# Optimization experiments

Hardware: AMD Instinct MI355X
Metric: run time of the kernel (lower is better)

## Reference

```python
import jax, jax.numpy as jnp
import numpy as np

NUM_HEADS = 16
HEAD_DIM = 64
BATCH = 4
SEQ = 1024
MAX_SEQ_LEN = 2048


def _shift(pos_score):
    # Transformer-XL relative shift. pos_score: (NH, S, S_kv)
    NH, S, S_kv = pos_score.shape
    zero_pad = jnp.zeros((NH, S, 1), dtype=pos_score.dtype)
    padded = jnp.concatenate([zero_pad, pos_score], axis=-1)  # (NH, S, S_kv+1)
    padded = padded.reshape(NH, S_kv + 1, S)
    return padded[:, 1:, :].reshape(NH, S, S_kv)


def setup_inputs() -> dict:
    key = jax.random.key(0)
    ks = jax.random.split(key, 6)
    NH = BATCH * NUM_HEADS
    return {
        "queries": jax.random.normal(ks[0], (NH, SEQ, HEAD_DIM), dtype=jnp.float32),
        "keys": jax.random.normal(ks[1], (NH, SEQ, HEAD_DIM), dtype=jnp.float32),
        "values": jax.random.normal(ks[2], (NH, SEQ, HEAD_DIM), dtype=jnp.float32),
        "u_bias": jax.random.normal(ks[3], (1, NUM_HEADS, 1, HEAD_DIM), dtype=jnp.float32),
        "v_bias": jax.random.normal(ks[4], (1, NUM_HEADS, 1, HEAD_DIM), dtype=jnp.float32),
        "R": jax.random.normal(ks[5], (NUM_HEADS, MAX_SEQ_LEN, HEAD_DIM), dtype=jnp.float32),
    }


def reference(queries, keys, values, u_bias, v_bias, R):
    NH, S, d = queries.shape
    S_kv = keys.shape[1]
    batch = NH // NUM_HEADS

    q = queries * (d ** -0.5)
    q = q.reshape(batch, NUM_HEADS, S, d)
    q_u = (q + u_bias).reshape(NH, S, d)
    q_v = (q + v_bias).reshape(NH, S, d)

    # relative position embeddings, tiled over batch: (NH, S_kv, d)
    R_s = jnp.tile(R[:, :S_kv, :], (batch, 1, 1))

    content_score = jnp.einsum('nsd,ntd->nst', q_u, keys)   # (NH, S, S_kv)
    pos_score = jnp.einsum('nsd,ntd->nst', q_v, R_s)        # (NH, S, S_kv)
    pos_score = _shift(pos_score)

    attn_weights = jax.nn.softmax(content_score + pos_score, axis=-1)
    attn = jnp.einsum('nst,ntd->nsd', attn_weights, values)  # (NH, S, d)
    return attn
```

## Files before the change

kernel.cpp:

```cpp
#include <hip/hip_runtime.h>


#define SQ    1024
#define HD    64
#define NHD   16
#define RMAX  2048

typedef _Float16 f16x8 __attribute__((ext_vector_type(8)));
typedef _Float16 f16x4 __attribute__((ext_vector_type(4)));
typedef short    b16x8 __attribute__((ext_vector_type(8)));
typedef float    f32x4 __attribute__((ext_vector_type(4)));

#define MFMA_F16(A,B,C)  __builtin_amdgcn_mfma_f32_16x16x32_f16((A),(B),(C),0,0,0)
#define MFMA_BF16(A,B,C) __builtin_amdgcn_mfma_f32_16x16x32_bf16((A),(B),(C),0,0,0)

#define KH_OFF   0
#define VT_OFF   (8u << 20)
#define R16_OFF  (18u << 20)
#define WS_NEED  (20u << 20)

__device__ __forceinline__ short f2b(float f) {
  unsigned u = __builtin_bit_cast(unsigned, f);
  u += 0x7FFFu + ((u >> 16) & 1u);
  return (short)(u >> 16);
}
__device__ __forceinline__ unsigned pkh(float a, float b) {
  _Float16 h0 = (_Float16)a, h1 = (_Float16)b;
  return (unsigned)__builtin_bit_cast(unsigned short, h0)
       | ((unsigned)__builtin_bit_cast(unsigned short, h1) << 16);
}


__global__ __launch_bounds__(256) void precvt_kr(
    const float* __restrict__ K, const float* __restrict__ R,
    _Float16* __restrict__ Kh, _Float16* __restrict__ R16)
{
  const int idx = blockIdx.x * 256 + threadIdx.x;
  const int nk4 = (64 * SQ * HD) / 4;
  if (idx < nk4) {
    float4 v = ((const float4*)K)[idx];
    f16x4 o = { (_Float16)v.x, (_Float16)v.y, (_Float16)v.z, (_Float16)v.w };
    *(f16x4*)(Kh + 4 * (size_t)idx) = o;
  } else {
    int rr = idx - nk4;
    int h  = rr >> 14, off = rr & 16383;
    float4 v = ((const float4*)R)[((size_t)h << 15) + off];
    f16x4 o = { (_Float16)v.x, (_Float16)v.y, (_Float16)v.z, (_Float16)v.w };
    *(f16x4*)(R16 + 4 * (((size_t)h << 14) + off)) = o;
  }
}

__global__ __launch_bounds__(256) void prevt_v(
    const float* __restrict__ V, short* __restrict__ Vt)
{
  __shared__ float t[64][65];
  const int n = blockIdx.x, st = blockIdx.y, tid = threadIdx.x;
  {
    const int row = tid >> 2, c0 = (tid & 3) * 16;
    const float* src = V + ((size_t)n * SQ + st * 64 + row) * HD + c0;
#pragma unroll
    for (int i = 0; i < 4; ++i) {
      float4 x = ((const float4*)src)[i];
      t[row][c0 + 4*i + 0] = x.x; t[row][c0 + 4*i + 1] = x.y;
      t[row][c0 + 4*i + 2] = x.z; t[row][c0 + 4*i + 3] = x.w;
    }
  }
  __syncthreads();
  {
    const int d = tid >> 2, s0 = (tid & 3) * 16;
    short* dst = Vt + ((size_t)n * 80 + d) * SQ + st * 64 + s0;
#pragma unroll
    for (int i = 0; i < 8; ++i) {
      unsigned pk = (unsigned)(unsigned short)f2b(t[s0 + 2*i][d])
                  | ((unsigned)(unsigned short)f2b(t[s0 + 2*i + 1][d]) << 16);
      *(unsigned*)(dst + 2*i) = pk;
    }
  }
  if (tid < 64) {
    const int s = st * 64 + tid;
    Vt[((size_t)n * 80 + 64) * SQ + s] = (short)0x3F80;
#pragma unroll
    for (int r = 65; r < 80; ++r) Vt[((size_t)n * 80 + r) * SQ + s] = 0;
  }
}


__global__ __launch_bounds__(256, 4) void relpos_sdpa_r5(
    const float* __restrict__ Q, const _Float16* __restrict__ Kh,
    const short* __restrict__ Vtg, const _Float16* __restrict__ R16,
    const float* __restrict__ Ub, const float* __restrict__ Vb,
    float* __restrict__ O)
{
  const int n    = blockIdx.x;
  const int h    = n & (NHD - 1);
  const int a0   = blockIdx.y * 64;
  const int tid  = threadIdx.x;
  const int lane = tid & 63, wave = tid >> 6;
  const int l15  = lane & 15, quad = lane >> 4;

  const float*    Qn  = Q   + (size_t)n * SQ * HD;
  const _Float16* Khn = Kh  + (size_t)n * SQ * HD;
  const short*    Vgn = Vtg + (size_t)n * 80 * SQ;
  const _Float16* Rh  = R16 + (size_t)h * SQ * HD;

  __shared__ __align__(16) char lds[38656];
  _Float16* Kb = (_Float16*)lds;
  short*    Ps = (short*)lds;
  short*    Vt = (short*)(lds + 9216);
  _Float16* Pb = (_Float16*)(lds + 9216 + 11520);

  f16x8 quF[2], qvF[5][2];
#pragma unroll
  for (int ks = 0; ks < 2; ++ks) {
    const int db = ks * 32 + quad * 8;
    float ub[8], vb[8];
#pragma unroll
    for (int j = 0; j < 8; ++j) { ub[j] = Ub[h*HD + db + j]; vb[j] = Vb[h*HD + db + j]; }
    {
      const float* p = Qn + (size_t)(a0 + 16*wave + l15) * HD + db;
      f16x8 f;
#pragma unroll
      for (int j = 0; j < 8; ++j) f[j] = (_Float16)(p[j] * 0.125f + ub[j]);
      quF[ks] = f;
    }
#pragma unroll
    for (int rt = 0; rt < 5; ++rt) {
      int row = a0 + 16*rt + l15; if (row > SQ-1) row = SQ-1;
      const float* p = Qn + (size_t)row * HD + db;
      f16x8 f;
#pragma unroll
      for (int j = 0; j < 8; ++j) f[j] = (_Float16)(p[j] * 0.125f + vb[j]);
      qvF[rt][ks] = f;
    }
  }

  if (tid < 64) Vt[64*72 + tid] = (short)0x3F80;

  f32x4 Oacc[5];
#pragma unroll
  for (int ct = 0; ct < 5; ++ct) Oacc[ct] = (f32x4){0.f, 0.f, 0.f, 0.f};

  auto band = [&](int jstart) {
    const int c    = jstart + 16*wave + l15;
    const int j    = (c + 2048) & (SQ - 1);
    const int slot = (c + 2048) & 127;
    const _Float16* rp = Rh + (size_t)j * HD + quad * 8;
    f16x8 B0 = *(const f16x8*)rp;
    f16x8 B1 = *(const f16x8*)(rp + 32);
#pragma unroll
    for (int rt = 0; rt < 5; ++rt) {
      f32x4 acc = (f32x4){0.f, 0.f, 0.f, 0.f};
      acc = MFMA_F16(qvF[rt][0], B0, acc);
      acc = MFMA_F16(qvF[rt][1], B1, acc);
      const int row = 16*rt + 4*quad;
      if (rt < 4) {
        *(unsigned*)&Pb[slot*70 + row]     = pkh(acc[0], acc[1]);
        *(unsigned*)&Pb[slot*70 + row + 2] = pkh(acc[2], acc[3]);
      } else if (quad == 0) {
        *(unsigned*)&Pb[slot*70 + row]     = pkh(acc[0], acc[1]);
      }
    }
  };

  band(-a0 - 65);
  band(-a0 - 1);

  const int sr = tid >> 2, sc4 = tid & 3;
  const int iiB = 16*wave + 4*quad;

  for (int k0 = 0; k0 < SQ; k0 += 64) {
    __syncthreads();

    {
      const _Float16* src = Khn + (size_t)(k0 + sr) * HD + sc4 * 16;
      *(f16x8*)&Kb[sr*72 + sc4*16]     = *(const f16x8*)src;
      *(f16x8*)&Kb[sr*72 + sc4*16 + 8] = *(const f16x8*)(src + 8);
    }
    {
      const short* src = Vgn + (size_t)sr * SQ + k0 + sc4 * 16;
      *(b16x8*)&Vt[sr*72 + sc4*16]     = *(const b16x8*)src;
      *(b16x8*)&Vt[sr*72 + sc4*16 + 8] = *(const b16x8*)(src + 8);
    }
    __syncthreads();

    f32x4 sc[4];
#pragma unroll
    for (int ct = 0; ct < 4; ++ct) {
      f16x8 b0 = *(const f16x8*)&Kb[(16*ct + l15)*72 + quad*8];
      f16x8 b1 = *(const f16x8*)&Kb[(16*ct + l15)*72 + 32 + quad*8];
      f32x4 acc = (f32x4){0.f, 0.f, 0.f, 0.f};
      acc = MFMA_F16(quF[0], b0, acc);
      acc = MFMA_F16(quF[1], b1, acc);
      sc[ct] = acc;
    }

    const int dlt = k0 - a0;
#pragma unroll
    for (int r = 0; r < 4; ++r) {
      const int ii = iiB + r;
#pragma unroll
      for (int ct = 0; ct < 4; ++ct) {
        const int e    = dlt + 16*ct + l15 - ii;
        const int u    = (e > 0) ? 1 : 0;
        const int slot = (e - 1 - u + 2048) & 127;
        float pos = (float)Pb[slot*70 + ii + u];
        float s   = sc[ct][r] + ((e == 1) ? 0.f : pos);
        sc[ct][r] = __expf(s - 40.0f);
      }
    }
    __syncthreads();

#pragma unroll
    for (int r = 0; r < 4; ++r)
#pragma unroll
      for (int ct = 0; ct < 4; ++ct)
        Ps[(iiB + r)*68 + 16*ct + l15] = f2b(sc[ct][r]);

    b16x8 pA0 = *(const b16x8*)&Ps[(16*wave + l15)*68 + quad*8];
    b16x8 pA1 = *(const b16x8*)&Ps[(16*wave + l15)*68 + 32 + quad*8];
#pragma unroll
    for (int ct = 0; ct < 5; ++ct) {
      b16x8 v0 = *(const b16x8*)&Vt[(16*ct + l15)*72 + quad*8];
      b16x8 v1 = *(const b16x8*)&Vt[(16*ct + l15)*72 + 32 + quad*8];
      Oacc[ct] = MFMA_BF16(pA0, v0, Oacc[ct]);
      Oacc[ct] = MFMA_BF16(pA1, v1, Oacc[ct]);
    }

    if (k0 < SQ - 64) band(k0 + 64 - a0 - 1);
  }

#pragma unroll
  for (int r = 0; r < 4; ++r) {
    float l   = __shfl(Oacc[4][r], lane & 48);
    float inv = 1.0f / l;
    const size_t rowo = (size_t)n * SQ * HD + (size_t)(a0 + iiB + r) * HD;
#pragma unroll
    for (int ct = 0; ct < 4; ++ct)
      O[rowo + 16*ct + l15] = Oacc[ct][r] * inv;
  }
}


__global__ __launch_bounds__(256, 4) void relpos_sdpa_r3(
    const float* __restrict__ Q, const float* __restrict__ K,
    const float* __restrict__ V, const float* __restrict__ Ub,
    const float* __restrict__ Vb, const float* __restrict__ R,
    float* __restrict__ O)
{
  const int n    = blockIdx.x;
  const int h    = n & (NHD - 1);
  const int a0   = blockIdx.y * 64;
  const int tid  = threadIdx.x;
  const int lane = tid & 63, wave = tid >> 6;
  const int l15  = lane & 15, quad = lane >> 4;

  const float* Qn = Q + (size_t)n * SQ * HD;
  const float* Kn = K + (size_t)n * SQ * HD;
  const float* Vn = V + (size_t)n * SQ * HD;
  const float* Rh = R + (size_t)h * RMAX * HD;

  __shared__ __align__(16) char lds[38656];
  _Float16* Kb = (_Float16*)lds;
  short*    Ps = (short*)lds;
  short*    Vt = (short*)(lds + 9216);
  _Float16* Pb = (_Float16*)(lds + 9216 + 11520);

  f16x8 quF[2], qvF[5][2];
#pragma unroll
  for (int ks = 0; ks < 2; ++ks) {
    const int db = ks * 32 + quad * 8;
    float ub[8], vb[8];
#pragma unroll
    for (int j = 0; j < 8; ++j) { ub[j] = Ub[h*HD + db + j]; vb[j] = Vb[h*HD + db + j]; }
    {
      const float* p = Qn + (size_t)(a0 + 16*wave + l15) * HD + db;
      f16x8 f;
#pragma unroll
      for (int j = 0; j < 8; ++j) f[j] = (_Float16)(p[j] * 0.125f + ub[j]);
      quF[ks] = f;
    }
#pragma unroll
    for (int rt = 0; rt < 5; ++rt) {
      int row = a0 + 16*rt + l15; if (row > SQ-1) row = SQ-1;
      const float* p = Qn + (size_t)row * HD + db;
      f16x8 f;
#pragma unroll
      for (int j = 0; j < 8; ++j) f[j] = (_Float16)(p[j] * 0.125f + vb[j]);
      qvF[rt][ks] = f;
    }
  }

  if (tid < 64) Vt[64*72 + tid] = (short)0x3F80;

  f32x4 Oacc[5];
#pragma unroll
  for (int ct = 0; ct < 5; ++ct) Oacc[ct] = (f32x4){0.f, 0.f, 0.f, 0.f};

  auto band = [&](int jstart) {
    const int c    = jstart + 16*wave + l15;
    const int j    = (c + 2048) & (SQ - 1);
    const int slot = (c + 2048) & 127;
    const float* rp = Rh + (size_t)j * HD + quad * 8;
    f16x8 B0, B1;
    {
      float4 x0 = *(const float4*)(rp),      x1 = *(const float4*)(rp + 4);
      float4 y0 = *(const float4*)(rp + 32), y1 = *(const float4*)(rp + 36);
#pragma unroll
      for (int t = 0; t < 4; ++t) { B0[t] = (_Float16)(&x0.x)[t]; B0[t+4] = (_Float16)(&x1.x)[t]; }
#pragma unroll
      for (int t = 0; t < 4; ++t) { B1[t] = (_Float16)(&y0.x)[t]; B1[t+4] = (_Float16)(&y1.x)[t]; }
    }
#pragma unroll
    for (int rt = 0; rt < 5; ++rt) {
      f32x4 acc = (f32x4){0.f, 0.f, 0.f, 0.f};
      acc = MFMA_F16(qvF[rt][0], B0, acc);
      acc = MFMA_F16(qvF[rt][1], B1, acc);
      const int row = 16*rt + 4*quad;
      if (rt < 4) {
        *(unsigned*)&Pb[slot*70 + row]     = pkh(acc[0], acc[1]);
        *(unsigned*)&Pb[slot*70 + row + 2] = pkh(acc[2], acc[3]);
      } else if (quad == 0) {
        *(unsigned*)&Pb[slot*70 + row]     = pkh(acc[0], acc[1]);
      }
    }
  };

  band(-a0 - 65);
  band(-a0 - 1);

  const int sr = tid >> 2, sc4 = tid & 3;
  const int iiB = 16*wave + 4*quad;

  for (int k0 = 0; k0 < SQ; k0 += 64) {
    __syncthreads();
    {
      const float* src = Kn + (size_t)(k0 + sr) * HD + sc4 * 16;
      float4 x0 = *(const float4*)(src),     x1 = *(const float4*)(src + 4);
      float4 y0 = *(const float4*)(src + 8), y1 = *(const float4*)(src + 12);
      f16x8 lo, hi;
#pragma unroll
      for (int t = 0; t < 4; ++t) { lo[t] = (_Float16)(&x0.x)[t]; lo[t+4] = (_Float16)(&x1.x)[t]; }
#pragma unroll
      for (int t = 0; t < 4; ++t) { hi[t] = (_Float16)(&y0.x)[t]; hi[t+4] = (_Float16)(&y1.x)[t]; }
      *(f16x8*)&Kb[sr*72 + sc4*16]     = lo;
      *(f16x8*)&Kb[sr*72 + sc4*16 + 8] = hi;
    }
    {
      const int g = lane >> 3;
#pragma unroll
      for (int i = 0; i < 8; ++i) {
        int bp = 8*wave + (i ^ g);
        float v0 = Vn[(size_t)(k0 + 2*bp)     * HD + lane];
        float v1 = Vn[(size_t)(k0 + 2*bp + 1) * HD + lane];
        unsigned pk = (unsigned)(unsigned short)f2b(v0)
                    | ((unsigned)(unsigned short)f2b(v1) << 16);
        *(unsigned*)&Vt[lane*72 + 2*bp] = pk;
      }
    }
    __syncthreads();

    f32x4 sc[4];
#pragma unroll
    for (int ct = 0; ct < 4; ++ct) {
      f16x8 b0 = *(const f16x8*)&Kb[(16*ct + l15)*72 + quad*8];
      f16x8 b1 = *(const f16x8*)&Kb[(16*ct + l15)*72 + 32 + quad*8];
      f32x4 acc = (f32x4){0.f, 0.f, 0.f, 0.f};
      acc = MFMA_F16(quF[0], b0, acc);
      acc = MFMA_F16(quF[1], b1, acc);
      sc[ct] = acc;
    }

    const int dlt = k0 - a0;
#pragma unroll
    for (int r = 0; r < 4; ++r) {
      const int ii = iiB + r;
#pragma unroll
      for (int ct = 0; ct < 4; ++ct) {
        const int e    = dlt + 16*ct + l15 - ii;
        const int u    = (e > 0) ? 1 : 0;
        const int slot = (e - 1 - u + 2048) & 127;
        float pos = (float)Pb[slot*70 + ii + u];
        float s   = sc[ct][r] + ((e == 1) ? 0.f : pos);
        sc[ct][r] = __expf(s - 40.0f);
      }
    }
    __syncthreads();

#pragma unroll
    for (int r = 0; r < 4; ++r)
#pragma unroll
      for (int ct = 0; ct < 4; ++ct)
        Ps[(iiB + r)*68 + 16*ct + l15] = f2b(sc[ct][r]);

    b16x8 pA0 = *(const b16x8*)&Ps[(16*wave + l15)*68 + quad*8];
    b16x8 pA1 = *(const b16x8*)&Ps[(16*wave + l15)*68 + 32 + quad*8];
#pragma unroll
    for (int ct = 0; ct < 5; ++ct) {
      b16x8 v0 = *(const b16x8*)&Vt[(16*ct + l15)*72 + quad*8];
      b16x8 v1 = *(const b16x8*)&Vt[(16*ct + l15)*72 + 32 + quad*8];
      Oacc[ct] = MFMA_BF16(pA0, v0, Oacc[ct]);
      Oacc[ct] = MFMA_BF16(pA1, v1, Oacc[ct]);
    }

    if (k0 < SQ - 64) band(k0 + 64 - a0 - 1);
  }

#pragma unroll
  for (int r = 0; r < 4; ++r) {
    float l   = __shfl(Oacc[4][r], lane & 48);
    float inv = 1.0f / l;
    const size_t rowo = (size_t)n * SQ * HD + (size_t)(a0 + iiB + r) * HD;
#pragma unroll
    for (int ct = 0; ct < 4; ++ct)
      O[rowo + 16*ct + l15] = Oacc[ct][r] * inv;
  }
}

extern "C" void kernel_launch(void* const* d_in, const int* in_sizes, int n_in,
                              void* d_out, int out_size, void* d_ws, size_t ws_size,
                              hipStream_t stream) {
  const float* Q  = (const float*)d_in[0];
  const float* K  = (const float*)d_in[1];
  const float* V  = (const float*)d_in[2];
  const float* Ub = (const float*)d_in[3];
  const float* Vb = (const float*)d_in[4];
  const float* R  = (const float*)d_in[5];
  float* O = (float*)d_out;

  if (ws_size >= WS_NEED) {
    _Float16* Kh  = (_Float16*)((char*)d_ws + KH_OFF);
    short*    Vt  = (short*)((char*)d_ws + VT_OFF);
    _Float16* R16 = (_Float16*)((char*)d_ws + R16_OFF);

    precvt_kr<<<5120, 256, 0, stream>>>(K, R, Kh, R16);
    prevt_v<<<dim3(64, 16), 256, 0, stream>>>(V, Vt);

    dim3 grid(64, 16);
    relpos_sdpa_r5<<<grid, 256, 0, stream>>>(Q, Kh, Vt, R16, Ub, Vb, O);
  } else {
    dim3 grid(64, 16);
    relpos_sdpa_r3<<<grid, 256, 0, stream>>>(Q, K, V, Ub, Vb, R, O);
  }
}
```

Measured before the change: 193.7 us.

## Merge preprocessing kernels and transpose positional score buffer layout in LDS

Fuses the K/R fp16 conversion and V transpose kernels into one launch, which removes a kernel launch and its gap. In the main kernel, the positional-score band buffer is re-laid out as row-pair-major packed half2 words with a stride of 132. This is meant to reduce LDS bank conflicts on the band writes and the gather reads, and it shrinks the LDS footprint slightly. The bf16 P stores now share a packing helper. The new gather indexing is more intricate and must stay correct across slot wraparound.

```diff
diff --git a/kernel.cpp b/kernel.cpp
--- a/kernel.cpp
+++ b/kernel.cpp
@@ -29,63 +29,65 @@
   return (unsigned)__builtin_bit_cast(unsigned short, h0)
        | ((unsigned)__builtin_bit_cast(unsigned short, h1) << 16);
 }
-
-
-__global__ __launch_bounds__(256) void precvt_kr(
+__device__ __forceinline__ unsigned pkb(float a, float b) {
+  return (unsigned)(unsigned short)f2b(a)
+       | ((unsigned)(unsigned short)f2b(b) << 16);
+}
+
+
+__global__ __launch_bounds__(256) void preprep(
     const float* __restrict__ K, const float* __restrict__ R,
-    _Float16* __restrict__ Kh, _Float16* __restrict__ R16)
-{
-  const int idx = blockIdx.x * 256 + threadIdx.x;
-  const int nk4 = (64 * SQ * HD) / 4;
-  if (idx < nk4) {
-    float4 v = ((const float4*)K)[idx];
-    f16x4 o = { (_Float16)v.x, (_Float16)v.y, (_Float16)v.z, (_Float16)v.w };
-    *(f16x4*)(Kh + 4 * (size_t)idx) = o;
-  } else {
-    int rr = idx - nk4;
-    int h  = rr >> 14, off = rr & 16383;
-    float4 v = ((const float4*)R)[((size_t)h << 15) + off];
-    f16x4 o = { (_Float16)v.x, (_Float16)v.y, (_Float16)v.z, (_Float16)v.w };
-    *(f16x4*)(R16 + 4 * (((size_t)h << 14) + off)) = o;
-  }
-}
-
-__global__ __launch_bounds__(256) void prevt_v(
-    const float* __restrict__ V, short* __restrict__ Vt)
+    const float* __restrict__ V,
+    _Float16* __restrict__ Kh, _Float16* __restrict__ R16,
+    short* __restrict__ Vt)
 {
   __shared__ float t[64][65];
-  const int n = blockIdx.x, st = blockIdx.y, tid = threadIdx.x;
-  {
-    const int row = tid >> 2, c0 = (tid & 3) * 16;
-    const float* src = V + ((size_t)n * SQ + st * 64 + row) * HD + c0;
-#pragma unroll
-    for (int i = 0; i < 4; ++i) {
-      float4 x = ((const float4*)src)[i];
-      t[row][c0 + 4*i + 0] = x.x; t[row][c0 + 4*i + 1] = x.y;
-      t[row][c0 + 4*i + 2] = x.z; t[row][c0 + 4*i + 3] = x.w;
-    }
-  }
-  __syncthreads();
-  {
-    const int d = tid >> 2, s0 = (tid & 3) * 16;
-    short* dst = Vt + ((size_t)n * 80 + d) * SQ + st * 64 + s0;
-#pragma unroll
-    for (int i = 0; i < 8; ++i) {
-      unsigned pk = (unsigned)(unsigned short)f2b(t[s0 + 2*i][d])
-                  | ((unsigned)(unsigned short)f2b(t[s0 + 2*i + 1][d]) << 16);
-      *(unsigned*)(dst + 2*i) = pk;
-    }
-  }
-  if (tid < 64) {
-    const int s = st * 64 + tid;
-    Vt[((size_t)n * 80 + 64) * SQ + s] = (short)0x3F80;
-#pragma unroll
-    for (int r = 65; r < 80; ++r) Vt[((size_t)n * 80 + r) * SQ + s] = 0;
-  }
-}
-
-
-__global__ __launch_bounds__(256, 4) void relpos_sdpa_r5(
+  const int bid = blockIdx.x, tid = threadIdx.x;
+  if (bid < 1024) {
+    const int n = bid >> 4, st = bid & 15;
+    {
+      const int row = tid >> 2, c0 = (tid & 3) * 16;
+      const float* src = V + ((size_t)n * SQ + st * 64 + row) * HD + c0;
+#pragma unroll
+      for (int i = 0; i < 4; ++i) {
+        float4 x = ((const float4*)src)[i];
+        t[row][c0 + 4*i + 0] = x.x; t[row][c0 + 4*i + 1] = x.y;
+        t[row][c0 + 4*i + 2] = x.z; t[row][c0 + 4*i + 3] = x.w;
+      }
+    }
+    __syncthreads();
+    {
+      const int d = tid >> 2, s0 = (tid & 3) * 16;
+      short* dst = Vt + ((size_t)n * 80 + d) * SQ + st * 64 + s0;
+#pragma unroll
+      for (int i = 0; i < 8; ++i)
+        *(unsigned*)(dst + 2*i) = pkb(t[s0 + 2*i][d], t[s0 + 2*i + 1][d]);
+    }
+    if (tid < 64) {
+      const int s = st * 64 + tid;
+      Vt[((size_t)n * 80 + 64) * SQ + s] = (short)0x3F80;
+#pragma unroll
+      for (int r = 65; r < 80; ++r) Vt[((size_t)n * 80 + r) * SQ + s] = 0;
+    }
+  } else {
+    const int idx = (bid - 1024) * 256 + tid;
+    const int nk4 = (64 * SQ * HD) / 4;
+    if (idx < nk4) {
+      float4 v = ((const float4*)K)[idx];
+      f16x4 o = { (_Float16)v.x, (_Float16)v.y, (_Float16)v.z, (_Float16)v.w };
+      *(f16x4*)(Kh + 4 * (size_t)idx) = o;
+    } else {
+      int rr = idx - nk4;
+      int h  = rr >> 14, off = rr & 16383;
+      float4 v = ((const float4*)R)[((size_t)h << 15) + off];
+      f16x4 o = { (_Float16)v.x, (_Float16)v.y, (_Float16)v.z, (_Float16)v.w };
+      *(f16x4*)(R16 + 4 * (((size_t)h << 14) + off)) = o;
+    }
+  }
+}
+
+
+__global__ __launch_bounds__(256, 4) void relpos_sdpa_r7(
     const float* __restrict__ Q, const _Float16* __restrict__ Kh,
     const short* __restrict__ Vtg, const _Float16* __restrict__ R16,
     const float* __restrict__ Ub, const float* __restrict__ Vb,
@@ -103,11 +105,12 @@
   const short*    Vgn = Vtg + (size_t)n * 80 * SQ;
   const _Float16* Rh  = R16 + (size_t)h * SQ * HD;
 
-  __shared__ __align__(16) char lds[38656];
-  _Float16* Kb = (_Float16*)lds;
-  short*    Ps = (short*)lds;
-  short*    Vt = (short*)(lds + 9216);
-  _Float16* Pb = (_Float16*)(lds + 9216 + 11520);
+  __shared__ __align__(16) char lds[38160];
+  _Float16* Kb  = (_Float16*)lds;
+  unsigned short* Ps = (unsigned short*)lds;
+  short*    Vt  = (short*)(lds + 9216);
+  unsigned* Pb2 = (unsigned*)(lds + 9216 + 11520);
+  const _Float16* Pb2h = (const _Float16*)Pb2;
 
   f16x8 quF[2], qvF[5][2];
 #pragma unroll
@@ -152,12 +155,12 @@
       f32x4 acc = (f32x4){0.f, 0.f, 0.f, 0.f};
       acc = MFMA_F16(qvF[rt][0], B0, acc);
       acc = MFMA_F16(qvF[rt][1], B1, acc);
-      const int row = 16*rt + 4*quad;
       if (rt < 4) {
-        *(unsigned*)&Pb[slot*70 + row]     = pkh(acc[0], acc[1]);
-        *(unsigned*)&Pb[slot*70 + row + 2] = pkh(acc[2], acc[3]);
+        const int rp0 = 8*rt + 2*quad;
+        Pb2[rp0*132 + slot]       = pkh(acc[0], acc[1]);
+        Pb2[(rp0 + 1)*132 + slot] = pkh(acc[2], acc[3]);
       } else if (quad == 0) {
-        *(unsigned*)&Pb[slot*70 + row]     = pkh(acc[0], acc[1]);
+        Pb2[32*132 + slot] = pkh(acc[0], acc[1]);
       }
     }
   };
@@ -198,12 +201,14 @@
 #pragma unroll
     for (int r = 0; r < 4; ++r) {
       const int ii = iiB + r;
+      const int adA = (ii >> 1) * 264 + (ii & 1);
+      const int adB = ((ii + 1) >> 1) * 264 + ((ii + 1) & 1);
 #pragma unroll
       for (int ct = 0; ct < 4; ++ct) {
         const int e    = dlt + 16*ct + l15 - ii;
         const int u    = (e > 0) ? 1 : 0;
-        const int slot = (e - 1 - u + 2048) & 127;
-        float pos = (float)Pb[slot*70 + ii + u];
+        const int slot = (e - 1 - u) & 127;
+        float pos = (float)Pb2h[(u ? adB : adA) + 2*slot];
         float s   = sc[ct][r] + ((e == 1) ? 0.f : pos);
         sc[ct][r] = __expf(s - 40.0f);
       }
@@ -211,10 +216,15 @@
     __syncthreads();
 
 #pragma unroll
-    for (int r = 0; r < 4; ++r)
-#pragma unroll
-      for (int ct = 0; ct < 4; ++ct)
-        Ps[(iiB + r)*68 + 16*ct + l15] = f2b(sc[ct][r]);
+    for (int r = 0; r < 4; ++r) {
+      unsigned w0 = pkb(sc[0][r], sc[1][r]);
+      unsigned w1 = pkb(sc[2][r], sc[3][r]);
+      const int pbase = (iiB + r)*68 + l15;
+      Ps[pbase]      = (unsigned short)w0;
+      Ps[pbase + 16] = (unsigned short)(w0 >> 16);
+      Ps[pbase + 32] = (unsigned short)w1;
+      Ps[pbase + 48] = (unsigned short)(w1 >> 16);
+    }
 
     b16x8 pA0 = *(const b16x8*)&Ps[(16*wave + l15)*68 + quad*8];
     b16x8 pA1 = *(const b16x8*)&Ps[(16*wave + l15)*68 + 32 + quad*8];
@@ -241,7 +251,7 @@
 }
 
 
-__global__ __launch_bounds__(256, 4) void relpos_sdpa_r3(
+__global__ __launch_bounds__(256, 4) void relpos_sdpa_fb(
     const float* __restrict__ Q, const float* __restrict__ K,
     const float* __restrict__ V, const float* __restrict__ Ub,
     const float* __restrict__ Vb, const float* __restrict__ R,
@@ -352,9 +362,7 @@
         int bp = 8*wave + (i ^ g);
         float v0 = Vn[(size_t)(k0 + 2*bp)     * HD + lane];
         float v1 = Vn[(size_t)(k0 + 2*bp + 1) * HD + lane];
-        unsigned pk = (unsigned)(unsigned short)f2b(v0)
-                    | ((unsigned)(unsigned short)f2b(v1) << 16);
-        *(unsigned*)&Vt[lane*72 + 2*bp] = pk;
+        *(unsigned*)&Vt[lane*72 + 2*bp] = pkb(v0, v1);
       }
     }
     __syncthreads();
@@ -432,13 +440,12 @@
     short*    Vt  = (short*)((char*)d_ws + VT_OFF);
     _Float16* R16 = (_Float16*)((char*)d_ws + R16_OFF);
 
-    precvt_kr<<<5120, 256, 0, stream>>>(K, R, Kh, R16);
-    prevt_v<<<dim3(64, 16), 256, 0, stream>>>(V, Vt);
+    preprep<<<6144, 256, 0, stream>>>(K, R, V, Kh, R16, Vt);
 
     dim3 grid(64, 16);
-    relpos_sdpa_r5<<<grid, 256, 0, stream>>>(Q, Kh, Vt, R16, Ub, Vb, O);
+    relpos_sdpa_r7<<<grid, 256, 0, stream>>>(Q, Kh, Vt, R16, Ub, Vb, O);
   } else {
     dim3 grid(64, 16);
-    relpos_sdpa_r3<<<grid, 256, 0, stream>>>(Q, K, V, Ub, Vb, R, O);
-  }
-}
+    relpos_sdpa_fb<<<grid, 256, 0, stream>>>(Q, K, V, Ub, Vb, R, O);
+  }
+}
```

Result: faster. 188.8 us (-2.5%).
